# Performance work log

Measured on AMD Instinct MI355X. Metric: run time of the kernel, lower is better.

The kernel has to match this reference:

```python
import jax, jax.numpy as jnp
import numpy as np

FEATURE_DIM = 4
K = 32            # num_instance: labels 0..K-1 (0 = background), all assumed present
DELTA_V = 0.5
DELTA_D = 1.5
LOSS_WEIGHT = 1.0
BG_SAMPLE = 100   # number of background pixels used in the bg discrimination term


def setup_inputs() -> dict:
    key = jax.random.key(0)
    k1, k2, k3 = jax.random.split(key, 3)
    B, H, W = 16, 640, 640
    emb = jax.random.normal(k1, (B, FEATURE_DIM, H, W), dtype=jnp.float32)
    instance = jax.random.randint(k2, (B, H, W), 0, K, dtype=jnp.int32)
    kernel = jnp.ones((B, H, W), jnp.float32)
    training_mask = jnp.ones((B, H, W), jnp.float32)
    bboxes = jnp.zeros((B, K, 4), jnp.float32)
    max_distances = jax.random.uniform(k3, (B, K), dtype=jnp.float32)
    return {"emb": emb, "instance": instance, "kernel": kernel,
            "training_mask": training_mask, "bboxes": bboxes,
            "max_distances": max_distances}


def _safe_norm(x, axis):
    # L2 norm with NaN-free gradient at 0 (needed for pairwise-mean diagonal)
    sq = jnp.sum(x * x, axis=axis)
    pos = sq > 0
    return jnp.where(pos, jnp.sqrt(jnp.where(pos, sq, 1.0)), 0.0)


def _forward_single(emb, instance, kernel, training_mask, max_distances):
    # emb: [D,H,W]; instance/kernel/training_mask: [H,W]; max_distances: [K]
    tm = (training_mask > 0.5).astype(jnp.int32)
    kn = (kernel > 0.5).astype(jnp.int32)
    inst2d = instance * tm
    inst = inst2d.reshape(-1)                       # [N]
    inst_k = (inst2d * kn).reshape(-1)              # [N] kernel-restricted labels
    e = emb.reshape(FEATURE_DIM, -1).T              # [N, D]
    ones = jnp.ones(e.shape[0], jnp.float32)

    # per-instance mean embedding over kernel region (segment mean)
    cnt_k = jax.ops.segment_sum(ones, inst_k, num_segments=K)
    sums = jax.ops.segment_sum(e, inst_k, num_segments=K)   # [K, D]
    mean = sums / jnp.maximum(cnt_k, 1.0)[:, None]
    mean = mean.at[0].set(0.0)   # torch never fills column for label 0

    # l_agg: pull every instance pixel toward its instance mean
    d = _safe_norm(e - mean[inst], axis=1)          # [N]
    scale = jnp.exp(max_distances)[inst]            # [N]
    val = jnp.log(jnp.maximum(scale * d - DELTA_V, 0.0) ** 2 + 1.0)
    cnt = jax.ops.segment_sum(ones, inst, num_segments=K)
    per_lbl = jax.ops.segment_sum(val, inst, num_segments=K) / jnp.maximum(cnt, 1.0)
    l_agg = jnp.mean(per_lbl[1:])

    # l_dis: push distinct instance means apart (exclude diag and label 0)
    coef = 1.0 - np.exp(-10.0 / K)
    pd = _safe_norm(mean[:, None, :] - mean[None, :, :], axis=-1)  # [K, K]
    pv = jnp.log(jnp.maximum(2.0 * DELTA_D - coef * pd, 0.0) ** 2 + 1.0)
    m = 1.0 - jnp.eye(K, dtype=jnp.float32)
    m = m.at[0, :].set(0.0).at[:, 0].set(0.0)
    sum_pair = jnp.sum(pv * m)

    # background term: BG_SAMPLE background pixels vs every instance mean
    # (stable argsort puts instance==0 pixels first -> deterministic selection)
    bg_idx = jnp.argsort((inst != 0).astype(jnp.int32))[:BG_SAMPLE]
    emb_bg = e[bg_idx]                               # [100, D]
    dbg = _safe_norm(emb_bg[None, :, :] - mean[:, None, :], axis=-1)  # [K, 100]
    vbg = jnp.log(jnp.maximum(2.0 * DELTA_D - coef * dbg, 0.0) ** 2 + 1.0)
    sum_bg = jnp.sum(jnp.mean(vbg, axis=1)[1:])

    l_dis = (sum_pair + sum_bg) / ((K - 1) * (K - 2) + (K - 1))
    l_reg = jnp.mean(jnp.log(_safe_norm(mean, axis=1) + 1.0)) * 0.001
    return l_agg + l_dis + l_reg


def reference(emb, instance, kernel, training_mask, bboxes, max_distances):
    loss = jax.vmap(_forward_single)(emb, instance, kernel, training_mask,
                                     max_distances)
    return LOSS_WEIGHT * jnp.mean(loss)
```

## Files before the change

### kernel.cpp

```cpp
#include <hip/hip_runtime.h>

#define KI 32
#define BG_SAMPLE 100


typedef __attribute__((ext_vector_type(8))) _Float16 half8;
typedef __attribute__((ext_vector_type(4))) float f32x4;
typedef __attribute__((ext_vector_type(4))) int i32x4;
typedef union { unsigned u[4]; half8 v; } hfrag;

static __device__ __forceinline__ unsigned pkrtz(float a, float b) {
  unsigned d;
  asm("v_cvt_pkrtz_f16_f32 %0, %1, %2" : "=v"(d) : "v"(a), "v"(b));
  return d;
}
static __device__ __forceinline__ unsigned ohpair16(int la, int lb_, int r) {
  return ((la == r) ? 0x3C00u : 0u) | ((lb_ == r) ? 0x3C000000u : 0u);
}
static __device__ __forceinline__ float waveReduceSum(float v) {
#pragma unroll
  for (int off = 32; off > 0; off >>= 1) v += __shfl_down(v, off, 64);
  return v;
}

#define EPAD 272

__global__ __launch_bounds__(256)
void pass1_kernel(const float* __restrict__ emb, const int* __restrict__ inst,
                  const float* __restrict__ kern, const float* __restrict__ tmask,
                  float* __restrict__ ws, int N, int bpb)
{
  const int b = blockIdx.y;
  const int t = threadIdx.x;
  const int lane = t & 63, w = t >> 6;
  const int c = lane & 15, g = lane >> 4;
  __shared__ int s_lab[4][256];
  __shared__ __align__(16) unsigned short s_embh[4][4 * EPAD];
  __shared__ float s_acc[160];
  for (int i = t; i < 160; i += 256) s_acc[i] = 0.f;
  __syncthreads();

  const size_t off = (size_t)b * N;
  const int*   instb = inst + off;
  const float* kernb = kern + off;
  const float* tmb   = tmask + off;
  const float* embb  = emb + (size_t)b * 4 * N;
  float* gout = ws + (size_t)b * 224;

  f32x4 acc0 = {0.f, 0.f, 0.f, 0.f};
  f32x4 acc1 = {0.f, 0.f, 0.f, 0.f};
  const int waves_total = bpb * 4;
  const int wave_id = blockIdx.x * 4 + w;
  const int tiles = N >> 8;

  int tile = wave_id;
  i32x4 L; f32x4 T, Kk, E0, E1, E2, E3;
  if (tile < tiles) {
    const int p0 = (tile << 8) + lane * 4;
    L  = __builtin_nontemporal_load((const i32x4*)(instb + p0));
    T  = __builtin_nontemporal_load((const f32x4*)(tmb + p0));
    Kk = __builtin_nontemporal_load((const f32x4*)(kernb + p0));
    E0 = *(const f32x4*)(embb + p0);
    E1 = *(const f32x4*)(embb + (size_t)N + p0);
    E2 = *(const f32x4*)(embb + (size_t)2 * N + p0);
    E3 = *(const f32x4*)(embb + (size_t)3 * N + p0);
  }
  while (tile < tiles) {
    int4 lb;
    lb.x = (T.x > 0.5f && Kk.x > 0.5f) ? L.x : 0;
    lb.y = (T.y > 0.5f && Kk.y > 0.5f) ? L.y : 0;
    lb.z = (T.z > 0.5f && Kk.z > 0.5f) ? L.z : 0;
    lb.w = (T.w > 0.5f && Kk.w > 0.5f) ? L.w : 0;
    *(int4*)&s_lab[w][lane * 4] = lb;
    uint2 r;
    r.x = pkrtz(E0.x, E0.y); r.y = pkrtz(E0.z, E0.w);
    *(uint2*)&s_embh[w][0 * EPAD + lane * 4] = r;
    r.x = pkrtz(E1.x, E1.y); r.y = pkrtz(E1.z, E1.w);
    *(uint2*)&s_embh[w][1 * EPAD + lane * 4] = r;
    r.x = pkrtz(E2.x, E2.y); r.y = pkrtz(E2.z, E2.w);
    *(uint2*)&s_embh[w][2 * EPAD + lane * 4] = r;
    r.x = pkrtz(E3.x, E3.y); r.y = pkrtz(E3.z, E3.w);
    *(uint2*)&s_embh[w][3 * EPAD + lane * 4] = r;

    const int next = tile + waves_total;
    if (next < tiles) {
      const int p0 = (next << 8) + lane * 4;
      L  = __builtin_nontemporal_load((const i32x4*)(instb + p0));
      T  = __builtin_nontemporal_load((const f32x4*)(tmb + p0));
      Kk = __builtin_nontemporal_load((const f32x4*)(kernb + p0));
      E0 = *(const f32x4*)(embb + p0);
      E1 = *(const f32x4*)(embb + (size_t)N + p0);
      E2 = *(const f32x4*)(embb + (size_t)2 * N + p0);
      E3 = *(const f32x4*)(embb + (size_t)3 * N + p0);
    }
#pragma unroll
    for (int j = 0; j < 8; ++j) {
      const int p8 = j * 32 + g * 8;
      const int4 l0 = *(const int4*)&s_lab[w][p8];
      const int4 l1 = *(const int4*)&s_lab[w][p8 + 4];
      hfrag fa0, fa1, fb;
      fa0.u[0] = ohpair16(l0.x, l0.y, c);
      fa0.u[1] = ohpair16(l0.z, l0.w, c);
      fa0.u[2] = ohpair16(l1.x, l1.y, c);
      fa0.u[3] = ohpair16(l1.z, l1.w, c);
      fa1.u[0] = ohpair16(l0.x, l0.y, c + 16);
      fa1.u[1] = ohpair16(l0.z, l0.w, c + 16);
      fa1.u[2] = ohpair16(l1.x, l1.y, c + 16);
      fa1.u[3] = ohpair16(l1.z, l1.w, c + 16);
      if (c < 4) {
        fb.v = *(const half8*)&s_embh[w][c * EPAD + p8];
      } else if (c == 4) {
        fb.u[0] = fb.u[1] = fb.u[2] = fb.u[3] = 0x3C003C00u;
      } else {
        fb.u[0] = fb.u[1] = fb.u[2] = fb.u[3] = 0u;
      }
      acc0 = __builtin_amdgcn_mfma_f32_16x16x32_f16(fa0.v, fb.v, acc0, 0, 0, 0);
      acc1 = __builtin_amdgcn_mfma_f32_16x16x32_f16(fa1.v, fb.v, acc1, 0, 0, 0);
    }
    tile = next;
  }

  if (c < 5) {
#pragma unroll
    for (int jj = 0; jj < 4; ++jj) {
      const int row = g * 4 + jj;
      atomicAdd(&s_acc[row * 5 + c], acc0[jj]);
      atomicAdd(&s_acc[(16 + row) * 5 + c], acc1[jj]);
    }
  }
  if ((N & 255) != 0 && blockIdx.x == 0) {
    for (int i = ((N >> 8) << 8) + t; i < N; i += 256) {
      int lab = (tmb[i] > 0.5f && kernb[i] > 0.5f) ? (instb[i] & 31) : 0;
      atomicAdd(&gout[32 + lab], 1.f);
      atomicAdd(&gout[64 + lab],  embb[i]);
      atomicAdd(&gout[96 + lab],  embb[(size_t)N + i]);
      atomicAdd(&gout[128 + lab], embb[(size_t)2 * N + i]);
      atomicAdd(&gout[160 + lab], embb[(size_t)3 * N + i]);
    }
  }
  __syncthreads();
  if (t < 160) {
    float v = s_acc[t];
    if (v != 0.f) {
      const int row = t / 5, cc = t % 5;
      if (cc < 4) atomicAdd(&gout[64 + cc * 32 + row], v);
      else        atomicAdd(&gout[32 + row], v);
    }
  }
}

__global__ __launch_bounds__(256)
void pass2_kernel(const float* __restrict__ emb, const int* __restrict__ inst,
                  const float* __restrict__ tmask, const float* __restrict__ maxd,
                  float* __restrict__ ws, int N, int B, int bpb)
{
  const int b = blockIdx.y;
  const int t = threadIdx.x;
  const int lane = t & 63, w = t >> 6;
  const int c = lane & 15, g = lane >> 4;
  __shared__ int s_lab[4][256];
  __shared__ __align__(16) unsigned short s_val[4][256];
  __shared__ __align__(16) float4 s_meanv[KI];
  __shared__ float s_scal[KI];
  __shared__ float s_acc[64];
  float* gacc = ws + (size_t)b * 224;
  if (t < KI) {
    float inv = (t == 0) ? 0.f : 1.0f / fmaxf(gacc[32 + t], 1.0f);
    float4 m;
    m.x = gacc[64 + t]  * inv;
    m.y = gacc[96 + t]  * inv;
    m.z = gacc[128 + t] * inv;
    m.w = gacc[160 + t] * inv;
    s_meanv[t] = m;
    s_scal[t] = expf(maxd[b * KI + t]);
  }
  for (int i = t; i < 64; i += 256) s_acc[i] = 0.f;
  __syncthreads();

  const size_t off = (size_t)b * N;
  const int*   instb = inst + off;
  const float* tmb   = tmask + off;
  const float* embb  = emb + (size_t)b * 4 * N;

  f32x4 acc0 = {0.f, 0.f, 0.f, 0.f};
  f32x4 acc1 = {0.f, 0.f, 0.f, 0.f};
  const int waves_total = bpb * 4;
  const int wave_id = blockIdx.x * 4 + w;
  const int tiles = N >> 8;

  int tile = wave_id;
  i32x4 L; f32x4 T, E0, E1, E2, E3;
  if (tile < tiles) {
    const int p0 = (tile << 8) + lane * 4;
    L  = __builtin_nontemporal_load((const i32x4*)(instb + p0));
    T  = __builtin_nontemporal_load((const f32x4*)(tmb + p0));
    E0 = *(const f32x4*)(embb + p0);
    E1 = *(const f32x4*)(embb + (size_t)N + p0);
    E2 = *(const f32x4*)(embb + (size_t)2 * N + p0);
    E3 = *(const f32x4*)(embb + (size_t)3 * N + p0);
  }
  while (tile < tiles) {
    int4 lb;
    lb.x = (T.x > 0.5f) ? (L.x & 31) : 0;
    lb.y = (T.y > 0.5f) ? (L.y & 31) : 0;
    lb.z = (T.z > 0.5f) ? (L.z & 31) : 0;
    lb.w = (T.w > 0.5f) ? (L.w & 31) : 0;
    *(int4*)&s_lab[w][lane * 4] = lb;
    float v0, v1, v2, v3;
#define VALC(res, li, a0, a1, a2, a3) {                                  \
      float4 mn = s_meanv[li];                                           \
      float sc = s_scal[li];                                             \
      float d0 = (a0) - mn.x, d1 = (a1) - mn.y;                          \
      float d2 = (a2) - mn.z, d3 = (a3) - mn.w;                          \
      float dd = sqrtf(d0 * d0 + d1 * d1 + d2 * d2 + d3 * d3);           \
      float aa = fmaxf(sc * dd - 0.5f, 0.f);                             \
      res = __logf(aa * aa + 1.f); }
    VALC(v0, lb.x, E0.x, E1.x, E2.x, E3.x)
    VALC(v1, lb.y, E0.y, E1.y, E2.y, E3.y)
    VALC(v2, lb.z, E0.z, E1.z, E2.z, E3.z)
    VALC(v3, lb.w, E0.w, E1.w, E2.w, E3.w)
#undef VALC
    uint2 vr;
    vr.x = pkrtz(v0, v1); vr.y = pkrtz(v2, v3);
    *(uint2*)&s_val[w][lane * 4] = vr;

    const int next = tile + waves_total;
    if (next < tiles) {
      const int p0 = (next << 8) + lane * 4;
      L  = __builtin_nontemporal_load((const i32x4*)(instb + p0));
      T  = __builtin_nontemporal_load((const f32x4*)(tmb + p0));
      E0 = *(const f32x4*)(embb + p0);
      E1 = *(const f32x4*)(embb + (size_t)N + p0);
      E2 = *(const f32x4*)(embb + (size_t)2 * N + p0);
      E3 = *(const f32x4*)(embb + (size_t)3 * N + p0);
    }
#pragma unroll
    for (int j = 0; j < 8; ++j) {
      const int p8 = j * 32 + g * 8;
      const int4 l0 = *(const int4*)&s_lab[w][p8];
      const int4 l1 = *(const int4*)&s_lab[w][p8 + 4];
      hfrag fa0, fa1, fb;
      fa0.u[0] = ohpair16(l0.x, l0.y, c);
      fa0.u[1] = ohpair16(l0.z, l0.w, c);
      fa0.u[2] = ohpair16(l1.x, l1.y, c);
      fa0.u[3] = ohpair16(l1.z, l1.w, c);
      fa1.u[0] = ohpair16(l0.x, l0.y, c + 16);
      fa1.u[1] = ohpair16(l0.z, l0.w, c + 16);
      fa1.u[2] = ohpair16(l1.x, l1.y, c + 16);
      fa1.u[3] = ohpair16(l1.z, l1.w, c + 16);
      if (c == 0) {
        fb.v = *(const half8*)&s_val[w][p8];
      } else if (c == 1) {
        fb.u[0] = fb.u[1] = fb.u[2] = fb.u[3] = 0x3C003C00u;
      } else {
        fb.u[0] = fb.u[1] = fb.u[2] = fb.u[3] = 0u;
      }
      acc0 = __builtin_amdgcn_mfma_f32_16x16x32_f16(fa0.v, fb.v, acc0, 0, 0, 0);
      acc1 = __builtin_amdgcn_mfma_f32_16x16x32_f16(fa1.v, fb.v, acc1, 0, 0, 0);
    }
    tile = next;
  }

  if (c < 2) {
#pragma unroll
    for (int jj = 0; jj < 4; ++jj) {
      const int row = g * 4 + jj;
      atomicAdd(&s_acc[c * 32 + row], acc0[jj]);
      atomicAdd(&s_acc[c * 32 + 16 + row], acc1[jj]);
    }
  }
  if ((N & 255) != 0 && blockIdx.x == 0) {
    for (int i = ((N >> 8) << 8) + t; i < N; i += 256) {
      int lab = (tmb[i] > 0.5f) ? (instb[i] & 31) : 0;
      float4 mn = s_meanv[lab];
      float sc = s_scal[lab];
      float d0 = embb[i] - mn.x;
      float d1 = embb[(size_t)N + i] - mn.y;
      float d2 = embb[(size_t)2 * N + i] - mn.z;
      float d3 = embb[(size_t)3 * N + i] - mn.w;
      float dd = sqrtf(d0 * d0 + d1 * d1 + d2 * d2 + d3 * d3);
      float aa = fmaxf(sc * dd - 0.5f, 0.f);
      atomicAdd(&gacc[192 + lab], __logf(aa * aa + 1.f));
      atomicAdd(&gacc[lab], 1.f);
    }
  }
  __syncthreads();
  if (t < 64) {
    float v = s_acc[t];
    if (v != 0.f) {
      if (t < 32) atomicAdd(&gacc[192 + t], v);
      else        atomicAdd(&gacc[t - 32], v);
    }
  }
}

__global__ __launch_bounds__(256)
void bg_kernel(const float* __restrict__ emb, const int* __restrict__ inst,
               const float* __restrict__ tmask, float* __restrict__ ws, int N, int B)
{
  const int b = blockIdx.x;
  const int t = threadIdx.x;
  const int lane = t & 63, wave = t >> 6;
  float* gacc = ws + (size_t)b * 224;
  __shared__ float mean[KI][4];
  __shared__ int s_bgidx[BG_SAMPLE];
  __shared__ int s_count;
  __shared__ int s_wcnt[4];
  if (t == 0) s_count = 0;
  if (t < KI) {
    float inv = (t == 0) ? 0.f : 1.0f / fmaxf(gacc[32 + t], 1.0f);
    mean[t][0] = gacc[64 + t]  * inv;
    mean[t][1] = gacc[96 + t]  * inv;
    mean[t][2] = gacc[128 + t] * inv;
    mean[t][3] = gacc[160 + t] * inv;
  }
  __syncthreads();
  const int*   instb = inst + (size_t)b * N;
  const float* tmb   = tmask + (size_t)b * N;

  for (int base = 0; base < N; base += 256) {
    if (s_count >= BG_SAMPLE) break;
    int i = base + t;
    bool p = false;
    if (i < N) {
      int lab = instb[i];
      if (tmb[i] <= 0.5f) lab = 0;
      p = (lab == 0);
    }
    unsigned long long m = __ballot(p);
    if (lane == 0) s_wcnt[wave] = __popcll(m);
    __syncthreads();
    int pos = s_count;
    for (int ww = 0; ww < wave; ++ww) pos += s_wcnt[ww];
    if (p) {
      pos += __popcll(m & ((1ull << lane) - 1ull));
      if (pos < BG_SAMPLE) s_bgidx[pos] = i;
    }
    __syncthreads();
    if (t == 0) s_count += s_wcnt[0] + s_wcnt[1] + s_wcnt[2] + s_wcnt[3];
    __syncthreads();
  }
  if (s_count < BG_SAMPLE) {
    for (int base = 0; base < N; base += 256) {
      if (s_count >= BG_SAMPLE) break;
      int i = base + t;
      bool p = false;
      if (i < N) {
        int lab = instb[i];
        if (tmb[i] <= 0.5f) lab = 0;
        p = (lab != 0);
      }
      unsigned long long m = __ballot(p);
      if (lane == 0) s_wcnt[wave] = __popcll(m);
      __syncthreads();
      int pos = s_count;
      for (int ww = 0; ww < wave; ++ww) pos += s_wcnt[ww];
      if (p) {
        pos += __popcll(m & ((1ull << lane) - 1ull));
        if (pos < BG_SAMPLE) s_bgidx[pos] = i;
      }
      __syncthreads();
      if (t == 0) s_count += s_wcnt[0] + s_wcnt[1] + s_wcnt[2] + s_wcnt[3];
      __syncthreads();
    }
  }
  __syncthreads();

  __shared__ float ebg[BG_SAMPLE][4];
  const float* embb = emb + (size_t)b * 4 * N;
  for (int j = t; j < BG_SAMPLE; j += 256) {
    int i = s_bgidx[j];
    ebg[j][0] = embb[i];
    ebg[j][1] = embb[(size_t)N + i];
    ebg[j][2] = embb[(size_t)2 * N + i];
    ebg[j][3] = embb[(size_t)3 * N + i];
  }
  __syncthreads();

  const float coef = 1.0f - expf(-10.0f / 32.0f);
  float lp = 0.f;
  for (int idx = t; idx < 31 * 31; idx += 256) {
    int i = 1 + idx / 31, j = 1 + idx % 31;
    if (i == j) continue;
    float d0 = mean[i][0] - mean[j][0];
    float d1 = mean[i][1] - mean[j][1];
    float d2 = mean[i][2] - mean[j][2];
    float d3 = mean[i][3] - mean[j][3];
    float pd = sqrtf(d0 * d0 + d1 * d1 + d2 * d2 + d3 * d3);
    float a = fmaxf(3.0f - coef * pd, 0.f);
    lp += logf(a * a + 1.f);
  }
  float lr = 0.f;
  for (int k = t; k < KI; k += 256) {
    float n = sqrtf(mean[k][0] * mean[k][0] + mean[k][1] * mean[k][1] +
                    mean[k][2] * mean[k][2] + mean[k][3] * mean[k][3]);
    lr += logf(n + 1.f);
  }
  float lbg = 0.f;
  for (int idx = t; idx < 31 * BG_SAMPLE; idx += 256) {
    int k = 1 + idx / BG_SAMPLE, j = idx % BG_SAMPLE;
    float d0 = ebg[j][0] - mean[k][0];
    float d1 = ebg[j][1] - mean[k][1];
    float d2 = ebg[j][2] - mean[k][2];
    float d3 = ebg[j][3] - mean[k][3];
    float dd = sqrtf(d0 * d0 + d1 * d1 + d2 * d2 + d3 * d3);
    float a = fmaxf(3.0f - coef * dd, 0.f);
    lbg += logf(a * a + 1.f);
  }
  float a0 = waveReduceSum(lp);
  float a1 = waveReduceSum(lr);
  float a2 = waveReduceSum(lbg);
  __shared__ float red[3][4];
  if (lane == 0) { red[0][wave] = a0; red[1][wave] = a1; red[2][wave] = a2; }
  __syncthreads();
  if (t == 0) {
    float* gmisc = ws + (size_t)B * 224 + (size_t)B * 128 + (size_t)b * 4;
    gmisc[0] = red[0][0] + red[0][1] + red[0][2] + red[0][3];
    gmisc[1] = (red[1][0] + red[1][1] + red[1][2] + red[1][3]) * (0.001f / 32.0f);
    gmisc[2] = (red[2][0] + red[2][1] + red[2][2] + red[2][3]) * (1.0f / BG_SAMPLE);
  }
}

__global__ __launch_bounds__(64)
void final_kernel(const float* __restrict__ ws, float* __restrict__ out, int B)
{
  const int t = threadIdx.x;
  __shared__ float s[64];
  float tot = 0.f;
  if (t < B) {
    const float* gacc  = ws + (size_t)t * 224;
    const float* gmisc = ws + (size_t)B * 224 + (size_t)B * 128 + (size_t)t * 4;
    float lagg = 0.f;
    for (int k = 1; k < KI; ++k)
      lagg += gacc[192 + k] / fmaxf(gacc[k], 1.0f);
    lagg *= (1.0f / 31.0f);
    float ldis = (gmisc[0] + gmisc[2]) * (1.0f / 961.0f);
    tot = lagg + ldis + gmisc[1];
  }
  s[t] = tot;
  __syncthreads();
  if (t == 0) {
    float sum = 0.f;
    for (int b = 0; b < B; ++b) sum += s[b];
    out[0] = sum / (float)B;
  }
}

extern "C" void kernel_launch(void* const* d_in, const int* in_sizes, int n_in,
                              void* d_out, int out_size, void* d_ws, size_t ws_size,
                              hipStream_t stream)
{
  const float* emb   = (const float*)d_in[0];
  const int*   inst  = (const int*)d_in[1];
  const float* kern  = (const float*)d_in[2];
  const float* tmask = (const float*)d_in[3];
  const float* maxd  = (const float*)d_in[5];
  float* out = (float*)d_out;
  float* ws  = (float*)d_ws;

  const int B = in_sizes[5] / KI;
  const int N = in_sizes[1] / B;
  const int bpb = 100;

  if (ws_size < (size_t)B * 356 * sizeof(float)) return;

  hipMemsetAsync(d_ws, 0, (size_t)B * 356 * sizeof(float), stream);
  pass1_kernel<<<dim3(bpb, B), 256, 0, stream>>>(emb, inst, kern, tmask, ws, N, bpb);
  pass2_kernel<<<dim3(bpb, B), 256, 0, stream>>>(emb, inst, tmask, maxd, ws, N, B, bpb);
  bg_kernel<<<B, 256, 0, stream>>>(emb, inst, tmask, ws, N, B);
  final_kernel<<<1, 64, 0, stream>>>(ws, out, B);
}
```

Measured before the change: 99.96 us.

## Cache fp16 embeddings and packed 8-bit labels from pass1 for pass2

```diff
diff --git a/kernel.cpp b/kernel.cpp
--- a/kernel.cpp
+++ b/kernel.cpp
@@ -8,6 +8,7 @@
 typedef __attribute__((ext_vector_type(4))) float f32x4;
 typedef __attribute__((ext_vector_type(4))) int i32x4;
 typedef union { unsigned u[4]; half8 v; } hfrag;
+typedef union { uint2 u; _Float16 h[4]; } h4u;
 
 static __device__ __forceinline__ unsigned pkrtz(float a, float b) {
   unsigned d;
@@ -26,9 +27,17 @@
 #define EPAD 272
 
 __global__ __launch_bounds__(256)
+void zero_kernel(float* __restrict__ ws, int n)
+{
+  int i = blockIdx.x * 256 + threadIdx.x;
+  if (i < n) ws[i] = 0.f;
+}
+
+__global__ __launch_bounds__(256)
 void pass1_kernel(const float* __restrict__ emb, const int* __restrict__ inst,
                   const float* __restrict__ kern, const float* __restrict__ tmask,
-                  float* __restrict__ ws, int N, int bpb)
+                  float* __restrict__ ws, unsigned short* __restrict__ e16,
+                  unsigned char* __restrict__ lab8, int N, int bpb)
 {
   const int b = blockIdx.y;
   const int t = threadIdx.x;
@@ -45,6 +54,8 @@
   const float* kernb = kern + off;
   const float* tmb   = tmask + off;
   const float* embb  = emb + (size_t)b * 4 * N;
+  unsigned short* e16b = e16 + (size_t)b * 4 * N;
+  unsigned* labg = (unsigned*)(lab8 + off);
   float* gout = ws + (size_t)b * 224;
 
   f32x4 acc0 = {0.f, 0.f, 0.f, 0.f};
@@ -60,38 +71,50 @@
     L  = __builtin_nontemporal_load((const i32x4*)(instb + p0));
     T  = __builtin_nontemporal_load((const f32x4*)(tmb + p0));
     Kk = __builtin_nontemporal_load((const f32x4*)(kernb + p0));
-    E0 = *(const f32x4*)(embb + p0);
-    E1 = *(const f32x4*)(embb + (size_t)N + p0);
-    E2 = *(const f32x4*)(embb + (size_t)2 * N + p0);
-    E3 = *(const f32x4*)(embb + (size_t)3 * N + p0);
+    E0 = __builtin_nontemporal_load((const f32x4*)(embb + p0));
+    E1 = __builtin_nontemporal_load((const f32x4*)(embb + (size_t)N + p0));
+    E2 = __builtin_nontemporal_load((const f32x4*)(embb + (size_t)2 * N + p0));
+    E3 = __builtin_nontemporal_load((const f32x4*)(embb + (size_t)3 * N + p0));
   }
   while (tile < tiles) {
+    const int p0 = (tile << 8) + lane * 4;
     int4 lb;
-    lb.x = (T.x > 0.5f && Kk.x > 0.5f) ? L.x : 0;
-    lb.y = (T.y > 0.5f && Kk.y > 0.5f) ? L.y : 0;
-    lb.z = (T.z > 0.5f && Kk.z > 0.5f) ? L.z : 0;
-    lb.w = (T.w > 0.5f && Kk.w > 0.5f) ? L.w : 0;
+    lb.x = (T.x > 0.5f && Kk.x > 0.5f) ? (L.x & 31) : 0;
+    lb.y = (T.y > 0.5f && Kk.y > 0.5f) ? (L.y & 31) : 0;
+    lb.z = (T.z > 0.5f && Kk.z > 0.5f) ? (L.z & 31) : 0;
+    lb.w = (T.w > 0.5f && Kk.w > 0.5f) ? (L.w & 31) : 0;
     *(int4*)&s_lab[w][lane * 4] = lb;
-    uint2 r;
-    r.x = pkrtz(E0.x, E0.y); r.y = pkrtz(E0.z, E0.w);
-    *(uint2*)&s_embh[w][0 * EPAD + lane * 4] = r;
-    r.x = pkrtz(E1.x, E1.y); r.y = pkrtz(E1.z, E1.w);
-    *(uint2*)&s_embh[w][1 * EPAD + lane * 4] = r;
-    r.x = pkrtz(E2.x, E2.y); r.y = pkrtz(E2.z, E2.w);
-    *(uint2*)&s_embh[w][2 * EPAD + lane * 4] = r;
-    r.x = pkrtz(E3.x, E3.y); r.y = pkrtz(E3.z, E3.w);
-    *(uint2*)&s_embh[w][3 * EPAD + lane * 4] = r;
+    unsigned lt;
+    lt  = (T.x > 0.5f) ? (unsigned)(L.x & 31) : 0u;
+    lt |= ((T.y > 0.5f) ? (unsigned)(L.y & 31) : 0u) << 8;
+    lt |= ((T.z > 0.5f) ? (unsigned)(L.z & 31) : 0u) << 16;
+    lt |= ((T.w > 0.5f) ? (unsigned)(L.w & 31) : 0u) << 24;
+    labg[(tile << 6) + lane] = lt;
+
+    uint2 r0, r1, r2, r3;
+    r0.x = pkrtz(E0.x, E0.y); r0.y = pkrtz(E0.z, E0.w);
+    r1.x = pkrtz(E1.x, E1.y); r1.y = pkrtz(E1.z, E1.w);
+    r2.x = pkrtz(E2.x, E2.y); r2.y = pkrtz(E2.z, E2.w);
+    r3.x = pkrtz(E3.x, E3.y); r3.y = pkrtz(E3.z, E3.w);
+    *(uint2*)&s_embh[w][0 * EPAD + lane * 4] = r0;
+    *(uint2*)&s_embh[w][1 * EPAD + lane * 4] = r1;
+    *(uint2*)&s_embh[w][2 * EPAD + lane * 4] = r2;
+    *(uint2*)&s_embh[w][3 * EPAD + lane * 4] = r3;
+    *(uint2*)(e16b + 0 * (size_t)N + p0) = r0;
+    *(uint2*)(e16b + 1 * (size_t)N + p0) = r1;
+    *(uint2*)(e16b + 2 * (size_t)N + p0) = r2;
+    *(uint2*)(e16b + 3 * (size_t)N + p0) = r3;
 
     const int next = tile + waves_total;
     if (next < tiles) {
-      const int p0 = (next << 8) + lane * 4;
-      L  = __builtin_nontemporal_load((const i32x4*)(instb + p0));
-      T  = __builtin_nontemporal_load((const f32x4*)(tmb + p0));
-      Kk = __builtin_nontemporal_load((const f32x4*)(kernb + p0));
-      E0 = *(const f32x4*)(embb + p0);
-      E1 = *(const f32x4*)(embb + (size_t)N + p0);
-      E2 = *(const f32x4*)(embb + (size_t)2 * N + p0);
-      E3 = *(const f32x4*)(embb + (size_t)3 * N + p0);
+      const int q0 = (next << 8) + lane * 4;
+      L  = __builtin_nontemporal_load((const i32x4*)(instb + q0));
+      T  = __builtin_nontemporal_load((const f32x4*)(tmb + q0));
+      Kk = __builtin_nontemporal_load((const f32x4*)(kernb + q0));
+      E0 = __builtin_nontemporal_load((const f32x4*)(embb + q0));
+      E1 = __builtin_nontemporal_load((const f32x4*)(embb + (size_t)N + q0));
+      E2 = __builtin_nontemporal_load((const f32x4*)(embb + (size_t)2 * N + q0));
+      E3 = __builtin_nontemporal_load((const f32x4*)(embb + (size_t)3 * N + q0));
     }
 #pragma unroll
     for (int j = 0; j < 8; ++j) {
@@ -130,12 +153,20 @@
   }
   if ((N & 255) != 0 && blockIdx.x == 0) {
     for (int i = ((N >> 8) << 8) + t; i < N; i += 256) {
-      int lab = (tmb[i] > 0.5f && kernb[i] > 0.5f) ? (instb[i] & 31) : 0;
+      int li = instb[i] & 31;
+      bool tm_ok = tmb[i] > 0.5f;
+      int lab = (tm_ok && kernb[i] > 0.5f) ? li : 0;
       atomicAdd(&gout[32 + lab], 1.f);
       atomicAdd(&gout[64 + lab],  embb[i]);
       atomicAdd(&gout[96 + lab],  embb[(size_t)N + i]);
       atomicAdd(&gout[128 + lab], embb[(size_t)2 * N + i]);
       atomicAdd(&gout[160 + lab], embb[(size_t)3 * N + i]);
+      lab8[off + i] = (unsigned char)(tm_ok ? li : 0);
+#pragma unroll
+      for (int d = 0; d < 4; ++d) {
+        _Float16 hv = (_Float16)embb[(size_t)d * N + i];
+        e16b[(size_t)d * N + i] = *(unsigned short*)&hv;
+      }
     }
   }
   __syncthreads();
@@ -150,8 +181,9 @@
 }
 
 __global__ __launch_bounds__(256)
-void pass2_kernel(const float* __restrict__ emb, const int* __restrict__ inst,
-                  const float* __restrict__ tmask, const float* __restrict__ maxd,
+void pass2_kernel(const unsigned short* __restrict__ e16,
+                  const unsigned char* __restrict__ lab8,
+                  const float* __restrict__ maxd,
                   float* __restrict__ ws, int N, int B, int bpb)
 {
   const int b = blockIdx.y;
@@ -178,9 +210,8 @@
   __syncthreads();
 
   const size_t off = (size_t)b * N;
-  const int*   instb = inst + off;
-  const float* tmb   = tmask + off;
-  const float* embb  = emb + (size_t)b * 4 * N;
+  const unsigned* labp = (const unsigned*)(lab8 + off);
+  const unsigned short* e16b = e16 + (size_t)b * 4 * N;
 
   f32x4 acc0 = {0.f, 0.f, 0.f, 0.f};
   f32x4 acc1 = {0.f, 0.f, 0.f, 0.f};
@@ -189,36 +220,37 @@
   const int tiles = N >> 8;
 
   int tile = wave_id;
-  i32x4 L; f32x4 T, E0, E1, E2, E3;
+  unsigned LT; uint2 H0, H1, H2, H3;
   if (tile < tiles) {
     const int p0 = (tile << 8) + lane * 4;
-    L  = __builtin_nontemporal_load((const i32x4*)(instb + p0));
-    T  = __builtin_nontemporal_load((const f32x4*)(tmb + p0));
-    E0 = *(const f32x4*)(embb + p0);
-    E1 = *(const f32x4*)(embb + (size_t)N + p0);
-    E2 = *(const f32x4*)(embb + (size_t)2 * N + p0);
-    E3 = *(const f32x4*)(embb + (size_t)3 * N + p0);
+    LT = labp[(tile << 6) + lane];
+    H0 = *(const uint2*)(e16b + 0 * (size_t)N + p0);
+    H1 = *(const uint2*)(e16b + 1 * (size_t)N + p0);
+    H2 = *(const uint2*)(e16b + 2 * (size_t)N + p0);
+    H3 = *(const uint2*)(e16b + 3 * (size_t)N + p0);
   }
   while (tile < tiles) {
     int4 lb;
-    lb.x = (T.x > 0.5f) ? (L.x & 31) : 0;
-    lb.y = (T.y > 0.5f) ? (L.y & 31) : 0;
-    lb.z = (T.z > 0.5f) ? (L.z & 31) : 0;
-    lb.w = (T.w > 0.5f) ? (L.w & 31) : 0;
+    lb.x = (int)(LT & 31u);
+    lb.y = (int)((LT >> 8) & 31u);
+    lb.z = (int)((LT >> 16) & 31u);
+    lb.w = (int)((LT >> 24) & 31u);
     *(int4*)&s_lab[w][lane * 4] = lb;
+    h4u c0, c1, c2, c3;
+    c0.u = H0; c1.u = H1; c2.u = H2; c3.u = H3;
     float v0, v1, v2, v3;
-#define VALC(res, li, a0, a1, a2, a3) {                                  \
+#define VALC(res, li, j) {                                               \
       float4 mn = s_meanv[li];                                           \
       float sc = s_scal[li];                                             \
-      float d0 = (a0) - mn.x, d1 = (a1) - mn.y;                          \
-      float d2 = (a2) - mn.z, d3 = (a3) - mn.w;                          \
+      float d0 = (float)c0.h[j] - mn.x, d1 = (float)c1.h[j] - mn.y;      \
+      float d2 = (float)c2.h[j] - mn.z, d3 = (float)c3.h[j] - mn.w;      \
       float dd = sqrtf(d0 * d0 + d1 * d1 + d2 * d2 + d3 * d3);           \
       float aa = fmaxf(sc * dd - 0.5f, 0.f);                             \
       res = __logf(aa * aa + 1.f); }
-    VALC(v0, lb.x, E0.x, E1.x, E2.x, E3.x)
-    VALC(v1, lb.y, E0.y, E1.y, E2.y, E3.y)
-    VALC(v2, lb.z, E0.z, E1.z, E2.z, E3.z)
-    VALC(v3, lb.w, E0.w, E1.w, E2.w, E3.w)
+    VALC(v0, lb.x, 0)
+    VALC(v1, lb.y, 1)
+    VALC(v2, lb.z, 2)
+    VALC(v3, lb.w, 3)
 #undef VALC
     uint2 vr;
     vr.x = pkrtz(v0, v1); vr.y = pkrtz(v2, v3);
@@ -226,13 +258,12 @@
 
     const int next = tile + waves_total;
     if (next < tiles) {
-      const int p0 = (next << 8) + lane * 4;
-      L  = __builtin_nontemporal_load((const i32x4*)(instb + p0));
-      T  = __builtin_nontemporal_load((const f32x4*)(tmb + p0));
-      E0 = *(const f32x4*)(embb + p0);
-      E1 = *(const f32x4*)(embb + (size_t)N + p0);
-      E2 = *(const f32x4*)(embb + (size_t)2 * N + p0);
-      E3 = *(const f32x4*)(embb + (size_t)3 * N + p0);
+      const int q0 = (next << 8) + lane * 4;
+      LT = labp[(next << 6) + lane];
+      H0 = *(const uint2*)(e16b + 0 * (size_t)N + q0);
+      H1 = *(const uint2*)(e16b + 1 * (size_t)N + q0);
+      H2 = *(const uint2*)(e16b + 2 * (size_t)N + q0);
+      H3 = *(const uint2*)(e16b + 3 * (size_t)N + q0);
     }
 #pragma unroll
     for (int j = 0; j < 8; ++j) {
@@ -271,13 +302,13 @@
   }
   if ((N & 255) != 0 && blockIdx.x == 0) {
     for (int i = ((N >> 8) << 8) + t; i < N; i += 256) {
-      int lab = (tmb[i] > 0.5f) ? (instb[i] & 31) : 0;
+      int lab = lab8[off + i] & 31;
       float4 mn = s_meanv[lab];
       float sc = s_scal[lab];
-      float d0 = embb[i] - mn.x;
-      float d1 = embb[(size_t)N + i] - mn.y;
-      float d2 = embb[(size_t)2 * N + i] - mn.z;
-      float d3 = embb[(size_t)3 * N + i] - mn.w;
+      float d0 = (float)(*(const _Float16*)&e16b[0 * (size_t)N + i]) - mn.x;
+      float d1 = (float)(*(const _Float16*)&e16b[1 * (size_t)N + i]) - mn.y;
+      float d2 = (float)(*(const _Float16*)&e16b[2 * (size_t)N + i]) - mn.z;
+      float d3 = (float)(*(const _Float16*)&e16b[3 * (size_t)N + i]) - mn.w;
       float dd = sqrtf(d0 * d0 + d1 * d1 + d2 * d2 + d3 * d3);
       float aa = fmaxf(sc * dd - 0.5f, 0.f);
       atomicAdd(&gacc[192 + lab], __logf(aa * aa + 1.f));
@@ -414,7 +445,7 @@
   if (lane == 0) { red[0][wave] = a0; red[1][wave] = a1; red[2][wave] = a2; }
   __syncthreads();
   if (t == 0) {
-    float* gmisc = ws + (size_t)B * 224 + (size_t)B * 128 + (size_t)b * 4;
+    float* gmisc = ws + (size_t)B * 224 + (size_t)b * 4;
     gmisc[0] = red[0][0] + red[0][1] + red[0][2] + red[0][3];
     gmisc[1] = (red[1][0] + red[1][1] + red[1][2] + red[1][3]) * (0.001f / 32.0f);
     gmisc[2] = (red[2][0] + red[2][1] + red[2][2] + red[2][3]) * (1.0f / BG_SAMPLE);
@@ -429,7 +460,7 @@
   float tot = 0.f;
   if (t < B) {
     const float* gacc  = ws + (size_t)t * 224;
-    const float* gmisc = ws + (size_t)B * 224 + (size_t)B * 128 + (size_t)t * 4;
+    const float* gmisc = ws + (size_t)B * 224 + (size_t)t * 4;
     float lagg = 0.f;
     for (int k = 1; k < KI; ++k)
       lagg += gacc[192 + k] / fmaxf(gacc[k], 1.0f);
@@ -462,11 +493,15 @@
   const int N = in_sizes[1] / B;
   const int bpb = 100;
 
-  if (ws_size < (size_t)B * 356 * sizeof(float)) return;
-
-  hipMemsetAsync(d_ws, 0, (size_t)B * 356 * sizeof(float), stream);
-  pass1_kernel<<<dim3(bpb, B), 256, 0, stream>>>(emb, inst, kern, tmask, ws, N, bpb);
-  pass2_kernel<<<dim3(bpb, B), 256, 0, stream>>>(emb, inst, tmask, maxd, ws, N, B, bpb);
+  const size_t accFloats = (size_t)B * 228;
+  unsigned short* e16 = (unsigned short*)(ws + accFloats);
+  unsigned char*  lab8 = (unsigned char*)(e16 + (size_t)B * 4 * N);
+  const size_t need = accFloats * 4 + (size_t)B * 4 * N * 2 + (size_t)B * N;
+  if (ws_size < need) return;
+
+  zero_kernel<<<(int)((accFloats + 255) / 256), 256, 0, stream>>>(ws, (int)accFloats);
+  pass1_kernel<<<dim3(bpb, B), 256, 0, stream>>>(emb, inst, kern, tmask, ws, e16, lab8, N, bpb);
+  pass2_kernel<<<dim3(bpb, B), 256, 0, stream>>>(e16, lab8, maxd, ws, N, B, bpb);
   bg_kernel<<<B, 256, 0, stream>>>(emb, inst, tmask, ws, N, B);
   final_kernel<<<1, 64, 0, stream>>>(ws, out, B);
 }
```

Measured after the change: 109.8 us. 1.1x slower.
